# Performance work log

Measured on AMD Instinct MI355X. Metric: run time of the kernel, lower is better.

Reference implementation:

```python
import jax, jax.numpy as jnp
import numpy as np

# dims: n=batch, T=n_shifts, dX=16, dU=8, H=256 hidden, L=128 ldim, K=64 n_aux (L=2K)

def setup_inputs() -> dict:
    key = jax.random.key(0)
    ks = jax.random.split(key, 16)
    n, T, dX, dU, H, L, K = 64, 64, 16, 8, 256, 128, 64
    def lin(k, fan_in, shape):
        return (jax.random.uniform(k, shape, jnp.float32) * 2.0 - 1.0) / np.sqrt(fan_in)
    xs = jax.random.normal(ks[0], (n, T, dX), jnp.float32)
    us = jax.random.normal(ks[1], (n, T - 1, dU), jnp.float32)
    theta = jax.random.uniform(ks[2], (K,), jnp.float32) * (2.0 * np.pi)
    inp = {
        'xs': xs, 'us': us,
        # stacked x-aux encoders (K copies): BN affine, 3 linear layers (last no bias), output scale
        'x_gamma': jnp.ones((K, dX)), 'x_beta': jnp.zeros((K, dX)),
        'xW1': lin(ks[3], dX, (K, dX, H)), 'xb1': jnp.zeros((K, H)),
        'xW2': lin(ks[4], H, (K, H, H)), 'xb2': jnp.zeros((K, H)),
        'xW3': lin(ks[5], H, (K, H, L)), 'x_scale': jnp.ones((K, L)),
        # stacked u-aux encoders (K copies)
        'u_gamma': jnp.ones((K, dU)), 'u_beta': jnp.zeros((K, dU)),
        'uW1': lin(ks[6], dU, (K, dU, H)), 'ub1': jnp.zeros((K, H)),
        'uW2': lin(ks[7], H, (K, H, H)), 'ub2': jnp.zeros((K, H)),
        'uW3': lin(ks[8], H, (K, H, L)), 'u_scale': jnp.ones((K, L)),
        # Jordan-block complex eigenvalues (|lam| ~ 0.95)
        'reL': 0.95 * jnp.cos(theta), 'imL': 0.95 * jnp.sin(theta),
        # decoder C: Linear(ldim, dim, bias=False) -> weight [dX, L]
        'C_W': lin(ks[9], L, (dX, L)),
    }
    return inp


def _encoder(x, gamma, beta, W1, b1, W2, b2, W3, scale):
    # x: [M, D]; stacked params over K nets. BN stats (training mode) are per-feature over M,
    # identical across nets since the same x feeds every net.
    mu = x.mean(0)
    var = ((x - mu) ** 2).mean(0)
    xn = (x - mu) * jax.lax.rsqrt(var + 1e-5)          # [M, D]
    h = xn[None] * gamma[:, None, :] + beta[:, None, :]  # [K, M, D]
    h = jax.nn.leaky_relu(jnp.einsum('kmd,kdh->kmh', h, W1) + b1[:, None, :])
    h = jax.nn.leaky_relu(jnp.einsum('kmd,kdh->kmh', h, W2) + b2[:, None, :])
    h = jnp.einsum('kmd,kdh->kmh', h, W3)               # last layer: no bias
    return h * scale[:, None, :]                        # [K, M, L]


def reference(xs, us, x_gamma, x_beta, xW1, xb1, xW2, xb2, xW3, x_scale,
              u_gamma, u_beta, uW1, ub1, uW2, ub2, uW3, u_scale, reL, imL, C_W):
    n, T, dX = xs.shape
    K = reL.shape[0]
    L = 2 * K
    Tm1 = T - 1
    # phi1s: [n, T, K(net), K(pair), 2]
    phi = _encoder(xs.reshape(n * T, dX), x_gamma, x_beta, xW1, xb1, xW2, xb2, xW3, x_scale)
    phi1s = jnp.moveaxis(phi, 0, 1).reshape(n, T, K, K, 2)
    # ures = psi(u) - psi(0): [n, T-1, K, K, 2]
    uflat = us.reshape(n * Tm1, -1)
    psi_u = _encoder(uflat, u_gamma, u_beta, uW1, ub1, uW2, ub2, uW3, u_scale)
    psi_0 = _encoder(jnp.zeros_like(uflat), u_gamma, u_beta, uW1, ub1, uW2, ub2, uW3, u_scale)
    ures = jnp.moveaxis(psi_u - psi_0, 0, 1).reshape(n, Tm1, K, K, 2)
    # block-diagonal Koopman: per net j a 2x2 rotation-scale [[re, im], [-im, re]]
    R = jnp.stack([jnp.stack([reL, imL], -1), jnp.stack([-imL, reL], -1)], -2)  # [K, 2, 2]

    def step(p, u_t):
        p = jnp.einsum('bjkc,jcd->bjkd', p + u_t, R)
        return p, p

    _, preds = jax.lax.scan(step, phi1s[:, 0], jnp.moveaxis(ures, 0, 1))
    preds = jnp.moveaxis(preds, 0, 1)  # [n, T-1, K, K, 2]

    def phi2y(p):
        # sum over net axis (-3), flatten pair dims -> [.., L], decode with C
        return p.sum(-3).reshape(*p.shape[:-3], L) @ C_W.T

    y = phi2y(phi1s[:, 1:])
    y_pred = phi2y(preds)
    return y, y_pred
```

## Files before the change

### kernel.cpp

```cpp
#include <hip/hip_runtime.h>

typedef __bf16 bf16_t;
typedef __bf16 bf16x8 __attribute__((ext_vector_type(8)));
typedef __bf16 bf16x4 __attribute__((ext_vector_type(4)));
typedef float  f32x4  __attribute__((ext_vector_type(4)));

__global__ __launch_bounds__(256) void prep_all_kernel(
    const float* __restrict__ xW1, const float* __restrict__ xb1,
    const float* __restrict__ xg,  const float* __restrict__ xbeta,
    const float* __restrict__ uW1, const float* __restrict__ ub1,
    const float* __restrict__ ug,  const float* __restrict__ ubeta,
    const float* __restrict__ xW2, const float* __restrict__ uW2,
    const float* __restrict__ xW3, const float* __restrict__ uW3,
    const float* __restrict__ x_scale, const float* __restrict__ u_scale,
    const float* __restrict__ ub2,
    const float* __restrict__ xs, const float* __restrict__ us,
    bf16_t* __restrict__ xW1t, float* __restrict__ xb1p,
    bf16_t* __restrict__ uW1t, float* __restrict__ ub1p,
    bf16_t* __restrict__ xW2t, bf16_t* __restrict__ uW2t,
    bf16_t* __restrict__ xW3t, bf16_t* __restrict__ uW3t,
    float* __restrict__ psi0, float* __restrict__ part)
{
    const int t = blockIdx.x, tid = threadIdx.x;
    __shared__ float tile[32][33];
    __shared__ float h1[256], h2[256];

    if (t < 12288) {
        const float* in; bf16_t* outp; const float* scale = nullptr;
        int j, r0, c0, C;
        if (t < 8192) {
            C = 256;
            j = (t & 4095) >> 6;
            const int tl = t & 63; r0 = (tl >> 3) * 32; c0 = (tl & 7) * 32;
            if (t < 4096) { in = xW2; outp = xW2t; }
            else          { in = uW2; outp = uW2t; }
        } else {
            C = 128;
            const int l = t - 8192;
            j = (l & 2047) >> 5;
            const int tl = l & 31; r0 = (tl >> 2) * 32; c0 = (tl & 3) * 32;
            if (l < 2048) { in = xW3; outp = xW3t; scale = x_scale + j * 128; }
            else          { in = uW3; outp = uW3t; scale = u_scale + j * 128; }
        }
        const int R = 256;
        in   += (size_t)j * R * C;
        bf16_t* op = outp + (size_t)j * R * C;
        const int tx = tid & 31, ty = tid >> 5;
        #pragma unroll
        for (int i = 0; i < 4; i++)
            tile[ty + i * 8][tx] = in[(size_t)(r0 + ty + i * 8) * C + c0 + tx];
        __syncthreads();
        #pragma unroll
        for (int i = 0; i < 4; i++) {
            int c = c0 + ty + i * 8;
            float sc = scale ? scale[c] : 1.f;
            op[(size_t)c * R + r0 + tx] = (bf16_t)(tile[tx][ty + i * 8] * sc);
        }
    } else if (t < 12416) {
        const int bid = t - 12288, j = bid & 63, h = tid;
        const float *W1, *b1, *gamma, *beta; bf16_t* W1t; float* b1p; int D;
        if (bid < 64) { W1 = xW1; b1 = xb1; gamma = xg; beta = xbeta; W1t = xW1t; b1p = xb1p; D = 16; }
        else          { W1 = uW1; b1 = ub1; gamma = ug; beta = ubeta; W1t = uW1t; b1p = ub1p; D = 8; }
        float bacc = b1[j * 256 + h];
        bf16_t* orow = W1t + (size_t)(j * 256 + h) * 32;
        for (int d = 0; d < 32; d++) orow[d] = (bf16_t)0.f;
        for (int d = 0; d < D; d++) {
            float w = W1[((size_t)j * D + d) * 256 + h];
            orow[d] = (bf16_t)(gamma[j * D + d] * w);
            bacc += beta[j * D + d] * w;
        }
        b1p[j * 256 + h] = bacc;
    } else if (t < 12480) {
        const int j = t - 12416, h = tid;
        {
            float bacc = ub1[j * 256 + h];
            #pragma unroll
            for (int d = 0; d < 8; d++)
                bacc += ubeta[j * 8 + d] * uW1[((size_t)j * 8 + d) * 256 + h];
            h1[h] = fmaxf(bacc, 0.01f * bacc);
        }
        __syncthreads();
        {
            float acc = ub2[j * 256 + h];
            const float* w2 = uW2 + (size_t)j * 65536 + h;
            #pragma unroll 8
            for (int d = 0; d < 256; d++) acc += h1[d] * w2[d * 256];
            h2[h] = fmaxf(acc, 0.01f * acc);
        }
        __syncthreads();
        if (h < 128) {
            float acc = 0.f;
            const float* w3 = uW3 + (size_t)j * 32768 + h;
            #pragma unroll 8
            for (int d = 0; d < 256; d++) acc += h2[d] * w3[d * 128];
            psi0[j * 128 + h] = acc * u_scale[j * 128 + h];
        }
    } else {
        const int bid = t - 12480;
        const bool isx = bid < 64;
        const float* x = isx ? xs : us;
        const int D   = isx ? 16 : 8;
        const int lb  = isx ? bid : bid - 64;
        const int per = isx ? 1024 : 1008;
        const int start = lb * per;
        float a = 0.f, b = 0.f;
        for (int idx = start + tid; idx < start + per; idx += 256) {
            float v = x[idx];
            a += v; b += v * v;
        }
        float* s1 = h1; float* s2 = h2;
        s1[tid] = a; s2[tid] = b;
        __syncthreads();
        if (tid < D) {
            float sa = 0.f, sb = 0.f;
            for (int k = tid; k < 256; k += D) { sa += s1[k]; sb += s2[k]; }
            part[bid * 32 + tid]      = sa;
            part[bid * 32 + 16 + tid] = sb;
        }
    }
}

__global__ __launch_bounds__(512, 4) void fused_mlp_kernel(
    const float* __restrict__ xs, const float* __restrict__ us,
    const float* __restrict__ part,
    const bf16_t* __restrict__ xW1t, const float* __restrict__ xb1p,
    const bf16_t* __restrict__ xW2t, const float* __restrict__ xb2,
    const bf16_t* __restrict__ xW3t,
    const bf16_t* __restrict__ uW1t, const float* __restrict__ ub1p,
    const bf16_t* __restrict__ uW2t, const float* __restrict__ ub2,
    const bf16_t* __restrict__ uW3t,
    bf16_t* __restrict__ phi, bf16_t* __restrict__ psiu)
{
    const int bid  = blockIdx.x;
    const int xcd  = bid & 7;
    const int slot = bid >> 3;
    const int band = slot >> 6;
    const int t64  = slot & 63;
    const int j    = xcd * 8 + band;
    const bool is_x = t64 < 32;
    const int tile  = is_x ? t64 : (t64 - 32);

    const float*  In  = is_x ? xs   : us;
    const int     D   = is_x ? 16   : 8;
    const bf16_t* W1t = is_x ? xW1t : uW1t;
    const float*  b1p = is_x ? xb1p : ub1p;
    const bf16_t* W2t = is_x ? xW2t : uW2t;
    const float*  b2  = is_x ? xb2  : ub2;
    const bf16_t* W3t = is_x ? xW3t : uW3t;
    bf16_t* outp      = is_x ? phi  : psiu;
    const int M       = is_x ? 4096 : 4032;

    const int row0 = tile * 128;
    const int tid  = threadIdx.x;
    const int wave = tid >> 6;
    const int lane = tid & 63;
    const int quad = lane >> 4;
    const int l16  = lane & 15;
    const int lo2  = l16 & 3, hi2 = l16 >> 2;

    __shared__ __align__(16) bf16_t hs[128 * 256];
    __shared__ float stats_s[32];

    if (tid < 16) {
        if (is_x) {
            float sa = 0.f, sb = 0.f;
            #pragma unroll 8
            for (int b = 0; b < 64; b++) { sa += part[b * 32 + tid]; sb += part[b * 32 + 16 + tid]; }
            float mu = sa / 4096.f, var = sb / 4096.f - mu * mu;
            stats_s[tid] = mu; stats_s[16 + tid] = rsqrtf(var + 1e-5f);
        } else if (tid < 8) {
            float sa = 0.f, sb = 0.f;
            #pragma unroll 8
            for (int b = 64; b < 96; b++) { sa += part[b * 32 + tid]; sb += part[b * 32 + 16 + tid]; }
            float mu = sa / 4032.f, var = sb / 4032.f - mu * mu;
            stats_s[tid] = mu; stats_s[16 + tid] = rsqrtf(var + 1e-5f);
        }
    }
    __syncthreads();

    const f32x4 vzero = {0.f, 0.f, 0.f, 0.f};

    char* const hsB = (char*)hs;
    const char* const abase = hsB + l16 * 512 + ((quad ^ lo2) << 4);
    const int  wlow0 = (quad >> 1) ^ lo2;
    char* const wbase = hsB + l16 * 512 + ((wave ^ hi2) << 6) + ((quad & 1) << 3);

    {
        bf16x8 wfr[2];
        #pragma unroll
        for (int nbi = 0; nbi < 2; nbi++)
            wfr[nbi] = *reinterpret_cast<const bf16x8*>(
                W1t + (size_t)(j * 256 + wave * 32 + nbi * 16 + l16) * 32 + quad * 8);

        f32x4 acc[8][2];
        #pragma unroll
        for (int a = 0; a < 8; a++) { acc[a][0] = vzero; acc[a][1] = vzero; }

        const int c0 = quad * 8;
        #pragma unroll
        for (int mb = 0; mb < 8; mb++) {
            bf16x8 a;
            if (c0 < D) {
                int row = row0 + mb * 16 + l16;
                if (row > M - 1) row = M - 1;
                const float* xp = In + (size_t)row * D + c0;
                f32x4 v0 = *reinterpret_cast<const f32x4*>(xp);
                f32x4 v1 = *reinterpret_cast<const f32x4*>(xp + 4);
                #pragma unroll
                for (int e = 0; e < 4; e++) a[e]     = (bf16_t)((v0[e] - stats_s[c0 + e])     * stats_s[16 + c0 + e]);
                #pragma unroll
                for (int e = 0; e < 4; e++) a[4 + e] = (bf16_t)((v1[e] - stats_s[c0 + 4 + e]) * stats_s[16 + c0 + 4 + e]);
            } else {
                #pragma unroll
                for (int e = 0; e < 8; e++) a[e] = (bf16_t)0.f;
            }
            #pragma unroll
            for (int nbi = 0; nbi < 2; nbi++)
                acc[mb][nbi] = __builtin_amdgcn_mfma_f32_16x16x32_bf16(
                    wfr[nbi], a, acc[mb][nbi], 0, 0, 0);
        }

        #pragma unroll
        for (int nbi = 0; nbi < 2; nbi++) {
            const f32x4 bias = *reinterpret_cast<const f32x4*>(
                b1p + j * 256 + wave * 32 + nbi * 16 + quad * 4);
            char* wp = wbase + ((wlow0 ^ (nbi << 1)) << 4);
            #pragma unroll
            for (int mb = 0; mb < 8; mb++) {
                bf16x4 pk;
                #pragma unroll
                for (int r = 0; r < 4; r++) {
                    float v = acc[mb][nbi][r] + bias[r];
                    v = fmaxf(v, 0.01f * v);
                    pk[r] = (bf16_t)v;
                }
                *reinterpret_cast<bf16x4*>(wp + mb * 8192) = pk;
            }
        }
    }
    __syncthreads();

    {
        f32x4 acc[8][2];
        #pragma unroll
        for (int a = 0; a < 8; a++) { acc[a][0] = vzero; acc[a][1] = vzero; }

        const bf16_t* w2base = W2t + ((size_t)j * 256 + wave * 32 + l16) * 256 + quad * 8;

        bf16x8 wr[3][2];
        #pragma unroll
        for (int d = 0; d < 3; d++)
            #pragma unroll
            for (int nbi = 0; nbi < 2; nbi++)
                wr[d][nbi] = *reinterpret_cast<const bf16x8*>(w2base + nbi * 4096 + d * 32);

        #pragma unroll
        for (int kk = 0; kk < 8; kk++) {
            const int c = kk % 3;
            const char* ap = abase + ((kk ^ hi2) << 6);
            bf16x8 av0[4];
            #pragma unroll
            for (int mb = 0; mb < 4; mb++)
                av0[mb] = *reinterpret_cast<const bf16x8*>(ap + mb * 8192);
            #pragma unroll
            for (int nbi = 0; nbi < 2; nbi++)
                #pragma unroll
                for (int mb = 0; mb < 4; mb++)
                    acc[mb][nbi] = __builtin_amdgcn_mfma_f32_16x16x32_bf16(
                        wr[c][nbi], av0[mb], acc[mb][nbi], 0, 0, 0);
            bf16x8 av1[4];
            #pragma unroll
            for (int mb = 0; mb < 4; mb++)
                av1[mb] = *reinterpret_cast<const bf16x8*>(ap + (mb + 4) * 8192);
            #pragma unroll
            for (int nbi = 0; nbi < 2; nbi++)
                #pragma unroll
                for (int mb = 4; mb < 8; mb++)
                    acc[mb][nbi] = __builtin_amdgcn_mfma_f32_16x16x32_bf16(
                        wr[c][nbi], av1[mb - 4], acc[mb][nbi], 0, 0, 0);
            if (kk < 5) {
                #pragma unroll
                for (int nbi = 0; nbi < 2; nbi++)
                    wr[c][nbi] = *reinterpret_cast<const bf16x8*>(
                        w2base + nbi * 4096 + (kk + 3) * 32);
            }
        }
        __syncthreads();
        #pragma unroll
        for (int nbi = 0; nbi < 2; nbi++) {
            const f32x4 bias = *reinterpret_cast<const f32x4*>(
                b2 + j * 256 + wave * 32 + nbi * 16 + quad * 4);
            char* wp = wbase + ((wlow0 ^ (nbi << 1)) << 4);
            #pragma unroll
            for (int mb = 0; mb < 8; mb++) {
                bf16x4 pk;
                #pragma unroll
                for (int r = 0; r < 4; r++) {
                    float v = acc[mb][nbi][r] + bias[r];
                    v = fmaxf(v, 0.01f * v);
                    pk[r] = (bf16_t)v;
                }
                *reinterpret_cast<bf16x4*>(wp + mb * 8192) = pk;
            }
        }
    }
    __syncthreads();

    {
        f32x4 acc[8];
        #pragma unroll
        for (int a = 0; a < 8; a++) acc[a] = vzero;

        const bf16_t* w3base = W3t + ((size_t)j * 128 + wave * 16 + l16) * 256 + quad * 8;

        bf16x8 wr[3];
        #pragma unroll
        for (int d = 0; d < 3; d++)
            wr[d] = *reinterpret_cast<const bf16x8*>(w3base + d * 32);

        #pragma unroll
        for (int kk = 0; kk < 8; kk++) {
            const int c = kk % 3;
            const char* ap = abase + ((kk ^ hi2) << 6);
            bf16x8 av0[4];
            #pragma unroll
            for (int mb = 0; mb < 4; mb++)
                av0[mb] = *reinterpret_cast<const bf16x8*>(ap + mb * 8192);
            #pragma unroll
            for (int mb = 0; mb < 4; mb++)
                acc[mb] = __builtin_amdgcn_mfma_f32_16x16x32_bf16(
                    wr[c], av0[mb], acc[mb], 0, 0, 0);
            bf16x8 av1[4];
            #pragma unroll
            for (int mb = 0; mb < 4; mb++)
                av1[mb] = *reinterpret_cast<const bf16x8*>(ap + (mb + 4) * 8192);
            #pragma unroll
            for (int mb = 4; mb < 8; mb++)
                acc[mb] = __builtin_amdgcn_mfma_f32_16x16x32_bf16(
                    wr[c], av1[mb - 4], acc[mb], 0, 0, 0);
            if (kk < 5)
                wr[c] = *reinterpret_cast<const bf16x8*>(w3base + (kk + 3) * 32);
        }
        __syncthreads();
        {
            const int sp3 = (wave * 2 + (quad >> 1)) ^ l16;
            char* w3p = hsB + l16 * 256 + sp3 * 16 + ((quad & 1) << 3);
            #pragma unroll
            for (int mb = 0; mb < 8; mb++) {
                bf16x4 pk;
                #pragma unroll
                for (int r = 0; r < 4; r++) pk[r] = (bf16_t)acc[mb][r];
                *reinterpret_cast<bf16x4*>(w3p + mb * 4096) = pk;
            }
        }
    }
    __syncthreads();
    #pragma unroll
    for (int p = 0; p < 4; p++) {
        const int rr = p * 32 + (tid >> 4);
        const int s  = tid & 15;
        if (row0 + rr < M) {
            bf16x8 v = *reinterpret_cast<const bf16x8*>(hs + rr * 128 + (s ^ (rr & 15)) * 8);
            *reinterpret_cast<bf16x8*>(outp + ((size_t)j * M + row0 + rr) * 128 + s * 8) = v;
        }
    }
}

__global__ __launch_bounds__(256) void y_kernel(
    const bf16_t* __restrict__ phi, const float* __restrict__ C_W,
    float* __restrict__ y) {
    const int m0 = blockIdx.x * 16;
    const int tid = threadIdx.x;
    __shared__ float S[16][128];
    __shared__ float Cs[2048];
    #pragma unroll
    for (int i = 0; i < 8; i++) Cs[tid + i * 256] = C_W[tid + i * 256];
    const int r  = tid >> 4;
    const int cg = (tid & 15) * 8;
    float acc[8];
    #pragma unroll
    for (int e = 0; e < 8; e++) acc[e] = 0.f;
    const bf16_t* p = phi + (size_t)(m0 + r) * 128 + cg;
    for (int j = 0; j < 64; j++) {
        bf16x8 v = *reinterpret_cast<const bf16x8*>(p + (size_t)j * 524288);
        #pragma unroll
        for (int e = 0; e < 8; e++) acc[e] += (float)v[e];
    }
    #pragma unroll
    for (int e = 0; e < 8; e++) S[r][cg + e] = acc[e];
    __syncthreads();
    const int mm = tid >> 4, o = tid & 15;
    const int m = m0 + mm;
    if ((m & 63) != 0) {
        float a = 0.f;
        #pragma unroll 8
        for (int l = 0; l < 128; l++) a += S[mm][l] * Cs[o * 128 + l];
        const int b = m >> 6, ti = (m & 63) - 1;
        y[(b * 63 + ti) * 16 + o] = a;
    }
}

__global__ __launch_bounds__(256) void scan_kernel(
    const bf16_t* __restrict__ phi, const bf16_t* __restrict__ psiu,
    const float* __restrict__ psi0, const float* __restrict__ reL,
    const float* __restrict__ imL, float* __restrict__ scratch) {
    const int b = blockIdx.x >> 3, jg = blockIdx.x & 7;
    const int tid = threadIdx.x;
    const int wave = tid >> 6, lane = tid & 63;
    __shared__ float red[2][4][128];

    const int j0 = jg * 8 + wave * 2;
    float sx0, sy0, sx1, sy1;
    float p0x0, p0y0, p0x1, p0y1, lre0, lim0, lre1, lim1;
    {
        unsigned v0 = *reinterpret_cast<const unsigned*>(
            phi + ((size_t)j0 * 4096 + b * 64) * 128 + lane * 2);
        unsigned v1 = *reinterpret_cast<const unsigned*>(
            phi + ((size_t)(j0 + 1) * 4096 + b * 64) * 128 + lane * 2);
        sx0 = __uint_as_float(v0 << 16); sy0 = __uint_as_float(v0 & 0xFFFF0000u);
        sx1 = __uint_as_float(v1 << 16); sy1 = __uint_as_float(v1 & 0xFFFF0000u);
        float2 p0 = *reinterpret_cast<const float2*>(psi0 + j0 * 128 + lane * 2);
        float2 p1 = *reinterpret_cast<const float2*>(psi0 + (j0 + 1) * 128 + lane * 2);
        p0x0 = p0.x; p0y0 = p0.y; p0x1 = p1.x; p0y1 = p1.y;
        lre0 = reL[j0]; lim0 = imL[j0]; lre1 = reL[j0 + 1]; lim1 = imL[j0 + 1];
    }
    const bf16_t* up0 = psiu + ((size_t)j0 * 4032 + b * 63) * 128 + lane * 2;
    const bf16_t* up1 = psiu + ((size_t)(j0 + 1) * 4032 + b * 63) * 128 + lane * 2;
    unsigned cur0 = *reinterpret_cast<const unsigned*>(up0);
    unsigned cur1 = *reinterpret_cast<const unsigned*>(up1);
    float* out = scratch + (size_t)blockIdx.x * 63 * 128;

    for (int t = 0; t < 63; t++) {
        unsigned nx0 = 0, nx1 = 0;
        if (t < 62) {
            nx0 = *reinterpret_cast<const unsigned*>(up0 + (t + 1) * 128);
            nx1 = *reinterpret_cast<const unsigned*>(up1 + (t + 1) * 128);
        }
        float px = sx0 + (__uint_as_float(cur0 << 16) - p0x0);
        float py = sy0 + (__uint_as_float(cur0 & 0xFFFF0000u) - p0y0);
        sx0 = px * lre0 - py * lim0;
        sy0 = px * lim0 + py * lre0;
        px = sx1 + (__uint_as_float(cur1 << 16) - p0x1);
        py = sy1 + (__uint_as_float(cur1 & 0xFFFF0000u) - p0y1);
        sx1 = px * lre1 - py * lim1;
        sy1 = px * lim1 + py * lre1;
        const int db = t & 1;
        red[db][wave][lane * 2]     = sx0 + sx1;
        red[db][wave][lane * 2 + 1] = sy0 + sy1;
        __syncthreads();
        if (tid < 128)
            out[t * 128 + tid] = red[db][0][tid] + red[db][1][tid]
                               + red[db][2][tid] + red[db][3][tid];
        cur0 = nx0; cur1 = nx1;
    }
}

__global__ __launch_bounds__(64) void decode_kernel(
    const float* __restrict__ scratch, const float* __restrict__ C_W,
    float* __restrict__ ypred) {
    const int t = blockIdx.x, b = blockIdx.y, l = threadIdx.x;
    __shared__ float S[128];
    float s0 = 0.f, s1 = 0.f;
    #pragma unroll
    for (int jg = 0; jg < 8; jg++) {
        float2 v = *reinterpret_cast<const float2*>(
            scratch + ((size_t)(b * 8 + jg) * 63 + t) * 128 + l * 2);
        s0 += v.x; s1 += v.y;
    }
    S[l * 2] = s0; S[l * 2 + 1] = s1;
    __syncthreads();
    const int o = l >> 2, q = l & 3;
    float acc = 0.f;
    #pragma unroll
    for (int i = 0; i < 32; i++)
        acc += S[q * 32 + i] * C_W[o * 128 + q * 32 + i];
    acc += __shfl_xor(acc, 2, 4);
    acc += __shfl_xor(acc, 1, 4);
    if (q == 0) ypred[(b * 63 + t) * 16 + o] = acc;
}

extern "C" void kernel_launch(void* const* d_in, const int* in_sizes, int n_in,
                              void* d_out, int out_size, void* d_ws, size_t ws_size,
                              hipStream_t stream) {
    const float* xs      = (const float*)d_in[0];
    const float* us      = (const float*)d_in[1];
    const float* x_gamma = (const float*)d_in[2];
    const float* x_beta  = (const float*)d_in[3];
    const float* xW1     = (const float*)d_in[4];
    const float* xb1     = (const float*)d_in[5];
    const float* xW2     = (const float*)d_in[6];
    const float* xb2     = (const float*)d_in[7];
    const float* xW3     = (const float*)d_in[8];
    const float* x_scale = (const float*)d_in[9];
    const float* u_gamma = (const float*)d_in[10];
    const float* u_beta  = (const float*)d_in[11];
    const float* uW1     = (const float*)d_in[12];
    const float* ub1     = (const float*)d_in[13];
    const float* uW2     = (const float*)d_in[14];
    const float* ub2     = (const float*)d_in[15];
    const float* uW3     = (const float*)d_in[16];
    const float* u_scale = (const float*)d_in[17];
    const float* reL     = (const float*)d_in[18];
    const float* imL     = (const float*)d_in[19];
    const float* C_W     = (const float*)d_in[20];

    char* ws = (char*)d_ws;
    size_t off = 0;
    auto alloc = [&](size_t bytes) -> char* {
        char* p = ws + off;
        off += (bytes + 255) & ~(size_t)255;
        return p;
    };
    float*  part = (float*)alloc(96 * 32 * 4);
    bf16_t* xW1t = (bf16_t*)alloc((size_t)64 * 256 * 32 * 2);
    float*  xb1p = (float*) alloc((size_t)64 * 256 * 4);
    bf16_t* xW2t = (bf16_t*)alloc((size_t)64 * 256 * 256 * 2);
    bf16_t* xW3t = (bf16_t*)alloc((size_t)64 * 128 * 256 * 2);
    bf16_t* uW1t = (bf16_t*)alloc((size_t)64 * 256 * 32 * 2);
    float*  ub1p = (float*) alloc((size_t)64 * 256 * 4);
    bf16_t* uW2t = (bf16_t*)alloc((size_t)64 * 256 * 256 * 2);
    bf16_t* uW3t = (bf16_t*)alloc((size_t)64 * 128 * 256 * 2);
    float*  psi0 = (float*) alloc((size_t)64 * 128 * 4);
    bf16_t* phi  = (bf16_t*)alloc((size_t)64 * 4096 * 128 * 2);
    bf16_t* psiu = (bf16_t*)alloc((size_t)64 * 4032 * 128 * 2);
    float*  scr  = (float*) alloc((size_t)512 * 63 * 128 * 4);

    float* y_out     = (float*)d_out;
    float* ypred_out = y_out + 64 * 63 * 16;

    prep_all_kernel<<<12576, 256, 0, stream>>>(
        xW1, xb1, x_gamma, x_beta, uW1, ub1, u_gamma, u_beta,
        xW2, uW2, xW3, uW3, x_scale, u_scale, ub2, xs, us,
        xW1t, xb1p, uW1t, ub1p, xW2t, uW2t, xW3t, uW3t, psi0, part);
    fused_mlp_kernel<<<4096, 512, 0, stream>>>(
        xs, us, part,
        xW1t, xb1p, xW2t, xb2, xW3t, uW1t, ub1p, uW2t, ub2, uW3t, phi, psiu);
    y_kernel<<<256, 256, 0, stream>>>(phi, C_W, y_out);
    scan_kernel<<<512, 256, 0, stream>>>(phi, psiu, psi0, reL, imL, scr);
    decode_kernel<<<dim3(63, 64), 64, 0, stream>>>(scr, C_W, ypred_out);
}
```

Measured before the change: 363.3 us.

## Retile layer-2/3 MFMA warps as 2x4 grid to cut LDS activation reads

Waves in the layer-2 and layer-3 GEMMs are regrouped from a 1-D split over output columns into a 2x4 grid, with two row halves and four column groups. Each wave now reads activations for only 64 rows but covers 64 (layer 2) or 32 (layer 3) output columns. This halves the LDS activation traffic per MFMA and raises reuse of the global weight fragments. Layer 2 also switches to a double-buffered weight prefetch one k-step ahead. The cost is more weight loads per wave and a different register footprint, with new swizzled store addresses for the intermediate activations.

```diff
diff --git a/kernel.cpp b/kernel.cpp
--- a/kernel.cpp
+++ b/kernel.cpp
@@ -157,6 +157,8 @@
     const int quad = lane >> 4;
     const int l16  = lane & 15;
     const int lo2  = l16 & 3, hi2 = l16 >> 2;
+    const int mh   = wave >> 2;
+    const int ng   = wave & 3;
 
     __shared__ __align__(16) bf16_t hs[128 * 256];
     __shared__ float stats_s[32];
@@ -181,9 +183,9 @@
     const f32x4 vzero = {0.f, 0.f, 0.f, 0.f};
 
     char* const hsB = (char*)hs;
-    const char* const abase = hsB + l16 * 512 + ((quad ^ lo2) << 4);
     const int  wlow0 = (quad >> 1) ^ lo2;
     char* const wbase = hsB + l16 * 512 + ((wave ^ hi2) << 6) + ((quad & 1) << 3);
+    const char* const abase2 = hsB + mh * 32768 + l16 * 512 + ((quad ^ lo2) << 4);
 
     {
         bf16x8 wfr[2];
@@ -241,58 +243,49 @@
     __syncthreads();
 
     {
-        f32x4 acc[8][2];
-        #pragma unroll
-        for (int a = 0; a < 8; a++) { acc[a][0] = vzero; acc[a][1] = vzero; }
-
-        const bf16_t* w2base = W2t + ((size_t)j * 256 + wave * 32 + l16) * 256 + quad * 8;
-
-        bf16x8 wr[3][2];
-        #pragma unroll
-        for (int d = 0; d < 3; d++)
-            #pragma unroll
-            for (int nbi = 0; nbi < 2; nbi++)
-                wr[d][nbi] = *reinterpret_cast<const bf16x8*>(w2base + nbi * 4096 + d * 32);
+        f32x4 acc[4][4];
+        #pragma unroll
+        for (int a = 0; a < 4; a++)
+            #pragma unroll
+            for (int b = 0; b < 4; b++) acc[a][b] = vzero;
+
+        const bf16_t* w2base = W2t + ((size_t)j * 256 + ng * 64 + l16) * 256 + quad * 8;
+
+        bf16x8 wr[2][4];
+        #pragma unroll
+        for (int nbi = 0; nbi < 4; nbi++)
+            wr[0][nbi] = *reinterpret_cast<const bf16x8*>(w2base + nbi * 4096);
 
         #pragma unroll
         for (int kk = 0; kk < 8; kk++) {
-            const int c = kk % 3;
-            const char* ap = abase + ((kk ^ hi2) << 6);
-            bf16x8 av0[4];
+            const int cur = kk & 1;
+            if (kk < 7) {
+                #pragma unroll
+                for (int nbi = 0; nbi < 4; nbi++)
+                    wr[cur ^ 1][nbi] = *reinterpret_cast<const bf16x8*>(
+                        w2base + nbi * 4096 + (kk + 1) * 32);
+            }
+            const char* ap = abase2 + ((kk ^ hi2) << 6);
+            bf16x8 av[4];
             #pragma unroll
             for (int mb = 0; mb < 4; mb++)
-                av0[mb] = *reinterpret_cast<const bf16x8*>(ap + mb * 8192);
-            #pragma unroll
-            for (int nbi = 0; nbi < 2; nbi++)
+                av[mb] = *reinterpret_cast<const bf16x8*>(ap + mb * 8192);
+            #pragma unroll
+            for (int nbi = 0; nbi < 4; nbi++)
                 #pragma unroll
                 for (int mb = 0; mb < 4; mb++)
                     acc[mb][nbi] = __builtin_amdgcn_mfma_f32_16x16x32_bf16(
-                        wr[c][nbi], av0[mb], acc[mb][nbi], 0, 0, 0);
-            bf16x8 av1[4];
-            #pragma unroll
-            for (int mb = 0; mb < 4; mb++)
-                av1[mb] = *reinterpret_cast<const bf16x8*>(ap + (mb + 4) * 8192);
-            #pragma unroll
-            for (int nbi = 0; nbi < 2; nbi++)
-                #pragma unroll
-                for (int mb = 4; mb < 8; mb++)
-                    acc[mb][nbi] = __builtin_amdgcn_mfma_f32_16x16x32_bf16(
-                        wr[c][nbi], av1[mb - 4], acc[mb][nbi], 0, 0, 0);
-            if (kk < 5) {
-                #pragma unroll
-                for (int nbi = 0; nbi < 2; nbi++)
-                    wr[c][nbi] = *reinterpret_cast<const bf16x8*>(
-                        w2base + nbi * 4096 + (kk + 3) * 32);
-            }
-        }
-        __syncthreads();
-        #pragma unroll
-        for (int nbi = 0; nbi < 2; nbi++) {
+                        wr[cur][nbi], av[mb], acc[mb][nbi], 0, 0, 0);
+        }
+        __syncthreads();
+        #pragma unroll
+        for (int nbi = 0; nbi < 4; nbi++) {
             const f32x4 bias = *reinterpret_cast<const f32x4*>(
-                b2 + j * 256 + wave * 32 + nbi * 16 + quad * 4);
-            char* wp = wbase + ((wlow0 ^ (nbi << 1)) << 4);
-            #pragma unroll
-            for (int mb = 0; mb < 8; mb++) {
+                b2 + j * 256 + ng * 64 + nbi * 16 + quad * 4);
+            char* wp = hsB + mh * 32768 + l16 * 512 + ((quad & 1) << 3)
+                     + ((((ng << 3) + (nbi << 1) + (quad >> 1)) ^ l16) << 4);
+            #pragma unroll
+            for (int mb = 0; mb < 4; mb++) {
                 bf16x4 pk;
                 #pragma unroll
                 for (int r = 0; r < 4; r++) {
@@ -307,50 +300,53 @@
     __syncthreads();
 
     {
-        f32x4 acc[8];
-        #pragma unroll
-        for (int a = 0; a < 8; a++) acc[a] = vzero;
-
-        const bf16_t* w3base = W3t + ((size_t)j * 128 + wave * 16 + l16) * 256 + quad * 8;
-
-        bf16x8 wr[3];
+        f32x4 acc[4][2];
+        #pragma unroll
+        for (int a = 0; a < 4; a++) { acc[a][0] = vzero; acc[a][1] = vzero; }
+
+        const bf16_t* w3base = W3t + ((size_t)j * 128 + ng * 32 + l16) * 256 + quad * 8;
+
+        bf16x8 wr[3][2];
         #pragma unroll
         for (int d = 0; d < 3; d++)
-            wr[d] = *reinterpret_cast<const bf16x8*>(w3base + d * 32);
+            #pragma unroll
+            for (int nbi = 0; nbi < 2; nbi++)
+                wr[d][nbi] = *reinterpret_cast<const bf16x8*>(w3base + nbi * 4096 + d * 32);
 
         #pragma unroll
         for (int kk = 0; kk < 8; kk++) {
             const int c = kk % 3;
-            const char* ap = abase + ((kk ^ hi2) << 6);
-            bf16x8 av0[4];
+            const char* ap = abase2 + ((kk ^ hi2) << 6);
+            bf16x8 av[4];
             #pragma unroll
             for (int mb = 0; mb < 4; mb++)
-                av0[mb] = *reinterpret_cast<const bf16x8*>(ap + mb * 8192);
-            #pragma unroll
-            for (int mb = 0; mb < 4; mb++)
-                acc[mb] = __builtin_amdgcn_mfma_f32_16x16x32_bf16(
-                    wr[c], av0[mb], acc[mb], 0, 0, 0);
-            bf16x8 av1[4];
-            #pragma unroll
-            for (int mb = 0; mb < 4; mb++)
-                av1[mb] = *reinterpret_cast<const bf16x8*>(ap + (mb + 4) * 8192);
-            #pragma unroll
-            for (int mb = 4; mb < 8; mb++)
-                acc[mb] = __builtin_amdgcn_mfma_f32_16x16x32_bf16(
-                    wr[c], av1[mb - 4], acc[mb], 0, 0, 0);
-            if (kk < 5)
-                wr[c] = *reinterpret_cast<const bf16x8*>(w3base + (kk + 3) * 32);
+                av[mb] = *reinterpret_cast<const bf16x8*>(ap + mb * 8192);
+            #pragma unroll
+            for (int nbi = 0; nbi < 2; nbi++)
+                #pragma unroll
+                for (int mb = 0; mb < 4; mb++)
+                    acc[mb][nbi] = __builtin_amdgcn_mfma_f32_16x16x32_bf16(
+                        wr[c][nbi], av[mb], acc[mb][nbi], 0, 0, 0);
+            if (kk < 5) {
+                #pragma unroll
+                for (int nbi = 0; nbi < 2; nbi++)
+                    wr[c][nbi] = *reinterpret_cast<const bf16x8*>(
+                        w3base + nbi * 4096 + (kk + 3) * 32);
+            }
         }
         __syncthreads();
         {
-            const int sp3 = (wave * 2 + (quad >> 1)) ^ l16;
-            char* w3p = hsB + l16 * 256 + sp3 * 16 + ((quad & 1) << 3);
-            #pragma unroll
-            for (int mb = 0; mb < 8; mb++) {
-                bf16x4 pk;
-                #pragma unroll
-                for (int r = 0; r < 4; r++) pk[r] = (bf16_t)acc[mb][r];
-                *reinterpret_cast<bf16x4*>(w3p + mb * 4096) = pk;
+            #pragma unroll
+            for (int nbi = 0; nbi < 2; nbi++) {
+                char* w3p = hsB + mh * 16384 + l16 * 256 + ((quad & 1) << 3)
+                          + ((((ng << 2) + (nbi << 1) + (quad >> 1)) ^ l16) << 4);
+                #pragma unroll
+                for (int mb = 0; mb < 4; mb++) {
+                    bf16x4 pk;
+                    #pragma unroll
+                    for (int r = 0; r < 4; r++) pk[r] = (bf16_t)acc[mb][nbi][r];
+                    *reinterpret_cast<bf16x4*>(w3p + mb * 4096) = pk;
+                }
             }
         }
     }
```

Measured after the change: 433.9 us. 19.4% more time.
